# Performance work log

Measured on AMD Instinct MI355X. Metric: run time of the kernel, lower is better.

Reference implementation:

```python
import jax, jax.numpy as jnp
import numpy as np
from jax import lax

B, N, C = 16, 2048, 128
NPOINT = 512
RADII = (0.1, 0.2, 0.4)
NSAMPLES = (16, 32, 48)
C_IN = C + 3          # use_xyz: relative xyz concatenated to features
C_OUT = 128
C_MID = C_OUT // 4    # mapping_func1 out channels (non-first-layer)


def fps(xyz, npoint):
    # sequential furthest point sampling; first index is 0 (matches CUDA FPS)
    b, n, _ = xyz.shape
    def step(carry, _):
        dist, last = carry
        p = xyz[jnp.arange(b), last]                    # (B,3) last selected point
        d = jnp.sum((xyz - p[:, None, :]) ** 2, -1)     # (B,N)
        dist = jnp.minimum(dist, d)
        nxt = jnp.argmax(dist, -1).astype(jnp.int32)
        return (dist, nxt), nxt
    idx0 = jnp.zeros((b,), jnp.int32)
    (_, _), rest = lax.scan(step, (jnp.full((b, n), 1e10, jnp.float32), idx0), None, length=npoint - 1)
    return jnp.concatenate([idx0[None], rest], 0).T     # (B,npoint)


def ball_query(xyz, new_xyz, radius, nsample):
    # first `nsample` in-ball indices (in original point order), pad with first hit
    n = xyz.shape[1]
    d2 = jnp.sum((new_xyz[:, :, None, :] - xyz[:, None, :, :]) ** 2, -1)  # (B,np,N)
    scores = jnp.where(d2 < radius * radius, jnp.arange(n, dtype=jnp.int32), n)
    vals = -lax.top_k(-scores, nsample)[0]               # ascending valid indices, invalid == n
    first = vals[..., :1]                                # center is always in its own ball
    return jnp.where(vals >= n, first, vals)             # (B,np,ns) int32


def gather_points(pts, idx):
    # pts (B,N,D), idx (B,np,ns) -> (B,np,ns,D)
    return jax.vmap(lambda p, i: p[i])(pts, idx)


def sa_forward(xyz, features, W1, b1, W2, b2, Wcr, bcr):
    fi = fps(xyz, NPOINT)
    new_xyz = jax.vmap(lambda p, i: p[i])(xyz, fi)       # (B,np,3)
    featT = jnp.transpose(features, (0, 2, 1))           # (B,N,C)
    outs = []
    for r, ns in zip(RADII, NSAMPLES):
        idx = ball_query(xyz, new_xyz, r, ns)
        g_xyz = gather_points(xyz, idx)                  # (B,np,ns,3) absolute neighbor coords
        rel = g_xyz - new_xyz[:, :, None, :]             # relative coords
        gf = gather_points(featT, idx)                   # (B,np,ns,C)
        x = jnp.concatenate([rel, gf], -1)               # (B,np,ns,C_in)
        dist = jnp.linalg.norm(rel, axis=-1, keepdims=True)
        ci = jnp.broadcast_to(new_xyz[:, :, None, :], g_xyz.shape)
        h10 = jnp.concatenate([dist, ci, g_xyz, rel], -1)        # relation prior (B,np,ns,10)
        h = jax.nn.relu(h10 @ W1 + b1) @ W2 + b2                 # dynamic weights (B,np,ns,C_in)
        pooled = jnp.max(jax.nn.relu(h * x), 2)                  # (B,np,C_in) max over neighbors
        outs.append(jax.nn.relu(pooled @ Wcr + bcr))             # channel raising (B,np,C_out)
    new_features = jnp.transpose(jnp.concatenate(outs, -1), (0, 2, 1))  # (B, 3*C_out, np)
    return new_xyz, new_features


def setup_inputs() -> dict:
    key = jax.random.key(0)
    ks = jax.random.split(key, 6)
    s = 0.05
    xyz = jax.random.uniform(ks[0], (B, N, 3), jnp.float32)
    features = jax.random.normal(ks[1], (B, C, N), jnp.float32)
    W1 = jax.random.normal(ks[2], (10, C_MID), jnp.float32) * s
    b1 = jnp.zeros((C_MID,), jnp.float32)
    W2 = jax.random.normal(ks[3], (C_MID, C_IN), jnp.float32) * s
    b2 = jnp.zeros((C_IN,), jnp.float32)
    Wcr = jax.random.normal(ks[4], (C_IN, C_OUT), jnp.float32) * s
    bcr = jnp.zeros((C_OUT,), jnp.float32)
    return dict(xyz=xyz, features=features, W1=W1, b1=b1, W2=W2, b2=b2, Wcr=Wcr, bcr=bcr)


def reference(xyz, features, W1, b1, W2, b2, Wcr, bcr):
    return sa_forward(xyz, features, W1, b1, W2, b2, Wcr, bcr)
```

## Files before the change

### kernel.cpp

```cpp
#include <hip/hip_runtime.h>
#include <hip/hip_bf16.h>

#define BATCH   16
#define NPTS    2048
#define NPOINT  512
#define CFEAT   128
#define CIN     131
#define CMID    32
#define NS_TOT  96

typedef float v2f __attribute__((ext_vector_type(2)));

__device__ __forceinline__ float d2_rn(float ax, float ay, float az,
                                       float bx, float by, float bz) {
  float dx = __fsub_rn(ax, bx), dy = __fsub_rn(ay, by), dz = __fsub_rn(az, bz);
  return __fadd_rn(__fadd_rn(__fmul_rn(dx, dx), __fmul_rn(dy, dy)), __fmul_rn(dz, dz));
}

__device__ __forceinline__ unsigned long long wave_kmax64(unsigned long long k) {
#define KSTEP(CTRL, RMASK, BMASK)                                              \
  {                                                                            \
    unsigned hi = (unsigned)(k >> 32), lo = (unsigned)k;                       \
    unsigned thi = (unsigned)__builtin_amdgcn_update_dpp(                      \
        (int)hi, (int)hi, CTRL, RMASK, BMASK, false);                          \
    unsigned tlo = (unsigned)__builtin_amdgcn_update_dpp(                      \
        (int)lo, (int)lo, CTRL, RMASK, BMASK, false);                          \
    unsigned long long tk = ((unsigned long long)thi << 32) | tlo;             \
    k = tk > k ? tk : k;                                                       \
  }
  KSTEP(0x111, 0xf, 0xf)
  KSTEP(0x112, 0xf, 0xf)
  KSTEP(0x114, 0xf, 0xe)
  KSTEP(0x118, 0xf, 0xc)
  KSTEP(0x142, 0xa, 0xf)
  KSTEP(0x143, 0xc, 0xf)
#undef KSTEP
  return k;
}

__global__ __launch_bounds__(256) void fps_transpose_kernel(
    const float* __restrict__ xyz, const float* __restrict__ feat,
    float* __restrict__ featT, float* __restrict__ out_xyz)
{
  int t = threadIdx.x;
  if (blockIdx.x >= BATCH) {
    __shared__ float tile[32][33];
    int m  = blockIdx.x - BATCH;
    int b  = m >> 8;
    int c0 = ((m >> 6) & 3) << 5;
    int n0 = (m & 63) << 5;
    int tx = t & 31, ty = t >> 5;
    const float* src = feat  + (size_t)b * CFEAT * NPTS;
    float*       dst = featT + (size_t)b * NPTS * CFEAT;
#pragma unroll
    for (int i = 0; i < 4; ++i)
      tile[ty + 8 * i][tx] = src[(size_t)(c0 + ty + 8 * i) * NPTS + n0 + tx];
    __syncthreads();
#pragma unroll
    for (int i = 0; i < 4; ++i)
      dst[(size_t)(n0 + ty + 8 * i) * CFEAT + c0 + tx] = tile[tx][ty + 8 * i];
    return;
  }
  __shared__ float4 sp[NPTS];
  __shared__ unsigned long long skey[2][4];
  __shared__ int slast[NPOINT];
  int b = blockIdx.x;
  const float* xb = xyz + (size_t)b * NPTS * 3;
  for (int n = t; n < NPTS; n += 256) {
    const float* p = xb + n * 3;
    sp[n] = make_float4(p[0], p[1], p[2], 0.f);
  }
  if (t == 0) slast[0] = 0;
  __syncthreads();
  float lx[8], ly[8], lz[8], d[8];
#pragma unroll
  for (int i = 0; i < 8; ++i) {
    float4 q = sp[(i << 8) + t];
    lx[i] = q.x; ly[i] = q.y; lz[i] = q.z;
    d[i] = 1e10f;
  }
  int last = 0;
  int w = t >> 6;
  int tb = 0xFFF - t;
#pragma unroll 1
  for (int step = 1; step < NPOINT; ++step) {
    float4 pv = sp[last];
    unsigned long long best = 0ull;
#pragma unroll
    for (int i = 0; i < 8; ++i) {
      float dd = d2_rn(lx[i], ly[i], lz[i], pv.x, pv.y, pv.z);
      float nd = fminf(d[i], dd);
      d[i] = nd;
      unsigned long long k = ((unsigned long long)__float_as_uint(nd) << 32)
                           | (unsigned)(tb - (i << 8));
      best = (k > best) ? k : best;
    }
    unsigned long long wk = wave_kmax64(best);
    int par = step & 1;
    if ((t & 63) == 63) skey[par][w] = wk;
    __syncthreads();
    unsigned long long k0 = skey[par][0], k1 = skey[par][1];
    unsigned long long k2 = skey[par][2], k3 = skey[par][3];
    unsigned long long ka = k0 > k1 ? k0 : k1;
    unsigned long long kb = k2 > k3 ? k2 : k3;
    unsigned long long km = ka > kb ? ka : kb;
    last = (0xFFF - (int)((unsigned)km & 0xFFFu)) & (NPTS - 1);
    if (t == 0) slast[step] = last;
  }
  __syncthreads();
  for (int s = t; s < NPOINT; s += 256) {
    float4 q = sp[slast[s]];
    float* o = out_xyz + ((size_t)b * NPOINT + s) * 3;
    o[0] = q.x; o[1] = q.y; o[2] = q.z;
  }
}

__global__ __launch_bounds__(128, 4) void center_kernel(
    const float* __restrict__ xyz, const float* __restrict__ featT,
    const float* __restrict__ W1, const float* __restrict__ b1,
    const float* __restrict__ W2, const float* __restrict__ b2,
    const float* __restrict__ Wcr, const float* __restrict__ bcr,
    const float* __restrict__ new_xyz, float* __restrict__ out_feat)
{
  int j = blockIdx.x, b = blockIdx.y, t = threadIdx.x;
  __shared__ int   sIdx[NS_TOT];
  __shared__ __align__(16) float sH1[NS_TOT * 36];
  __shared__ float sVr[NS_TOT * 4];
  __shared__ __align__(16) float sPooled[3 * 132];

  float cx = new_xyz[((size_t)b * NPOINT + j) * 3 + 0];
  float cy = new_xyz[((size_t)b * NPOINT + j) * 3 + 1];
  float cz = new_xyz[((size_t)b * NPOINT + j) * 3 + 2];

  {
    int w = t >> 6, lane = t & 63;
    const float* xb = xyz + (size_t)b * NPTS * 3;
    unsigned long long lt = (1ull << lane) - 1ull;
    if (w == 0) {
      int c0 = 0, c1 = 0;
      for (int it = 0; it < 32; ++it) {
        int n = (it << 6) + lane;
        float px = xb[n * 3 + 0], py = xb[n * 3 + 1], pz = xb[n * 3 + 2];
        float d2 = d2_rn(cx, cy, cz, px, py, pz);
        bool i0 = d2 < 0.01f, i1 = d2 < 0.04f;
        unsigned long long m0 = __ballot(i0), m1 = __ballot(i1);
        if (i0) { int pos = c0 + __popcll(m0 & lt); if (pos < 16) sIdx[pos] = n; }
        if (i1) { int pos = c1 + __popcll(m1 & lt); if (pos < 32) sIdx[16 + pos] = n; }
        c0 += __popcll(m0); c1 += __popcll(m1);
        if (c0 >= 16 && c1 >= 32) break;
      }
      int f0 = sIdx[0];
      int f1 = sIdx[16];
      if (lane >= c0 && lane < 16) sIdx[lane] = f0;
      if (lane >= c1 && lane < 32) sIdx[16 + lane] = f1;
    } else {
      int c2 = 0;
      for (int it = 0; it < 32; ++it) {
        int n = (it << 6) + lane;
        float px = xb[n * 3 + 0], py = xb[n * 3 + 1], pz = xb[n * 3 + 2];
        float d2 = d2_rn(cx, cy, cz, px, py, pz);
        bool i2 = d2 < 0.16f;
        unsigned long long m2 = __ballot(i2);
        if (i2) { int pos = c2 + __popcll(m2 & lt); if (pos < 48) sIdx[48 + pos] = n; }
        c2 += __popcll(m2);
        if (c2 >= 48) break;
      }
      int f2 = sIdx[48];
      if (lane >= c2 && lane < 48) sIdx[48 + lane] = f2;
    }
  }
  __syncthreads();

  if (t < NS_TOT) {
    int idx = sIdx[t];
    const float* p = xyz + ((size_t)b * NPTS + (size_t)idx) * 3;
    float px = p[0], py = p[1], pz = p[2];
    float rx = __fsub_rn(px, cx), ry = __fsub_rn(py, cy), rz = __fsub_rn(pz, cz);
    float dist = sqrtf(__fadd_rn(__fadd_rn(__fmul_rn(rx, rx), __fmul_rn(ry, ry)),
                                 __fmul_rn(rz, rz)));
    float h10[10] = {dist, cx, cy, cz, px, py, pz, rx, ry, rz};
    float h1r[CMID];
#pragma unroll
    for (int m = 0; m < CMID / 2; ++m) {
      v2f a = { b1[2 * m], b1[2 * m + 1] };
#pragma unroll
      for (int i = 0; i < 10; ++i) {
        v2f wv = { W1[i * CMID + 2 * m], W1[i * CMID + 2 * m + 1] };
        v2f hv = { h10[i], h10[i] };
        a = __builtin_elementwise_fma(hv, wv, a);
      }
      v2f z = { 0.f, 0.f };
      a = __builtin_elementwise_max(a, z);
      h1r[2 * m] = a.x; h1r[2 * m + 1] = a.y;
    }
#pragma unroll
    for (int q = 0; q < 8; ++q)
      *(float4*)&sH1[t * 36 + 4 * q] = *(const float4*)&h1r[4 * q];
    v2f pa0 = { b2[0], 0.f }, pa1 = { b2[1], 0.f }, pa2 = { b2[2], 0.f };
#pragma unroll
    for (int m = 0; m < CMID / 2; ++m) {
      v2f hv = { h1r[2 * m], h1r[2 * m + 1] };
      v2f w0 = { W2[(2 * m) * CIN + 0], W2[(2 * m + 1) * CIN + 0] };
      v2f w1 = { W2[(2 * m) * CIN + 1], W2[(2 * m + 1) * CIN + 1] };
      v2f w2 = { W2[(2 * m) * CIN + 2], W2[(2 * m + 1) * CIN + 2] };
      pa0 = __builtin_elementwise_fma(hv, w0, pa0);
      pa1 = __builtin_elementwise_fma(hv, w1, pa1);
      pa2 = __builtin_elementwise_fma(hv, w2, pa2);
    }
    float a0 = __fadd_rn(pa0.x, pa0.y);
    float a1 = __fadd_rn(pa1.x, pa1.y);
    float a2 = __fadd_rn(pa2.x, pa2.y);
    sVr[t * 4 + 0] = fmaxf(__fmul_rn(a0, rx), 0.f);
    sVr[t * 4 + 1] = fmaxf(__fmul_rn(a1, ry), 0.f);
    sVr[t * 4 + 2] = fmaxf(__fmul_rn(a2, rz), 0.f);
  }
  __syncthreads();

  {
    int w = t >> 6, lane = t & 63;
    v2f wA[16], wB[16];
#pragma unroll
    for (int m = 0; m < 16; ++m) {
      wA[m] = (v2f){ W2[(2 * m) * CIN + 3 + lane],
                     W2[(2 * m + 1) * CIN + 3 + lane] };
      wB[m] = (v2f){ W2[(2 * m) * CIN + 3 + lane + 64],
                     W2[(2 * m + 1) * CIN + 3 + lane + 64] };
    }
    float bA = b2[3 + lane], bB = b2[3 + lane + 64];
    const float* ftb = featT + (size_t)b * NPTS * CFEAT;
    int sBeg = w ? 48 : 0;
    int sEnd = w ? 96 : 48;
    int sMid = w ? 10000 : 16;
    float xA0 = ftb[(size_t)sIdx[sBeg] * CFEAT + lane];
    float xB0 = ftb[(size_t)sIdx[sBeg] * CFEAT + lane + 64];
    float xA1 = ftb[(size_t)sIdx[sBeg + 1] * CFEAT + lane];
    float xB1 = ftb[(size_t)sIdx[sBeg + 1] * CFEAT + lane + 64];
    float plA = 0.f, plB = 0.f;
#pragma unroll 1
    for (int s = sBeg; s < sEnd; ++s) {
      int sp2 = (s + 2 < sEnd) ? s + 2 : sEnd - 1;
      float xA2 = ftb[(size_t)sIdx[sp2] * CFEAT + lane];
      float xB2 = ftb[(size_t)sIdx[sp2] * CFEAT + lane + 64];
      const float4* h4 = (const float4*)&sH1[s * 36];
      v2f aAA = (v2f){ bA, 0.f }, aAB = (v2f){ 0.f, 0.f };
      v2f aBA = (v2f){ bB, 0.f }, aBB = (v2f){ 0.f, 0.f };
#pragma unroll
      for (int q = 0; q < 8; ++q) {
        float4 h = h4[q];
        v2f hxy = (v2f){ h.x, h.y }, hzw = (v2f){ h.z, h.w };
        aAA = __builtin_elementwise_fma(hxy, wA[2 * q],     aAA);
        aAB = __builtin_elementwise_fma(hzw, wA[2 * q + 1], aAB);
        aBA = __builtin_elementwise_fma(hxy, wB[2 * q],     aBA);
        aBB = __builtin_elementwise_fma(hzw, wB[2 * q + 1], aBB);
      }
      float hA = __fadd_rn(__fadd_rn(aAA.x, aAA.y), __fadd_rn(aAB.x, aAB.y));
      float hB = __fadd_rn(__fadd_rn(aBA.x, aBA.y), __fadd_rn(aBB.x, aBB.y));
      plA = fmaxf(plA, fmaxf(__fmul_rn(hA, xA0), 0.f));
      plB = fmaxf(plB, fmaxf(__fmul_rn(hB, xB0), 0.f));
      xA0 = xA1; xA1 = xA2; xB0 = xB1; xB1 = xB2;
      if (s + 1 == sMid) {
        sPooled[0 * 132 + 3 + lane]      = plA;
        sPooled[0 * 132 + 3 + lane + 64] = plB;
        plA = 0.f; plB = 0.f;
      }
    }
    int rowL = w ? 2 : 1;
    sPooled[rowL * 132 + 3 + lane]      = plA;
    sPooled[rowL * 132 + 3 + lane + 64] = plB;
  }
  if (t < 9) {
    int r = t / 3, c = t - r * 3;
    int s0 = (r == 0) ? 0 : (r == 1 ? 16 : 48);
    int s1 = (r == 0) ? 16 : (r == 1 ? 48 : 96);
    float pl = 0.f;
    for (int s = s0; s < s1; ++s) pl = fmaxf(pl, sVr[s * 4 + c]);
    sPooled[r * 132 + c] = pl;
  }
  __syncthreads();

  v2f s01 = { bcr[t], bcr[t] };
  float s2 = bcr[t];
#pragma unroll 1
  for (int k4 = 0; k4 < 128; k4 += 4) {
    float4 p0 = *(const float4*)&sPooled[k4];
    float4 p1 = *(const float4*)&sPooled[132 + k4];
    float4 p2 = *(const float4*)&sPooled[264 + k4];
#pragma unroll
    for (int u = 0; u < 4; ++u) {
      float w = Wcr[(k4 + u) * CFEAT + t];
      float e0 = (&p0.x)[u], e1 = (&p1.x)[u], e2 = (&p2.x)[u];
      s01 = __builtin_elementwise_fma((v2f){ e0, e1 }, (v2f){ w, w }, s01);
      s2  = fmaf(e2, w, s2);
    }
  }
#pragma unroll
  for (int k = 128; k < CIN; ++k) {
    float w = Wcr[k * CFEAT + t];
    s01 = __builtin_elementwise_fma((v2f){ sPooled[k], sPooled[132 + k] },
                                    (v2f){ w, w }, s01);
    s2  = fmaf(sPooled[264 + k], w, s2);
  }
  float* ob = out_feat + (size_t)b * 384 * NPOINT + j;
  ob[(size_t)(0 * CFEAT + t) * NPOINT] = fmaxf(s01.x, 0.f);
  ob[(size_t)(1 * CFEAT + t) * NPOINT] = fmaxf(s01.y, 0.f);
  ob[(size_t)(2 * CFEAT + t) * NPOINT] = fmaxf(s2, 0.f);
}

extern "C" void kernel_launch(void* const* d_in, const int* in_sizes, int n_in,
                              void* d_out, int out_size, void* d_ws, size_t ws_size,
                              hipStream_t stream) {
  const float* xyz  = (const float*)d_in[0];
  const float* feat = (const float*)d_in[1];
  const float* W1   = (const float*)d_in[2];
  const float* b1   = (const float*)d_in[3];
  const float* W2   = (const float*)d_in[4];
  const float* b2   = (const float*)d_in[5];
  const float* Wcr  = (const float*)d_in[6];
  const float* bcr  = (const float*)d_in[7];
  float* out_xyz  = (float*)d_out;
  float* out_feat = out_xyz + (size_t)BATCH * NPOINT * 3;
  float* featT    = (float*)d_ws;

  fps_transpose_kernel<<<BATCH + BATCH * 256, 256, 0, stream>>>(xyz, feat, featT, out_xyz);
  center_kernel<<<dim3(NPOINT, BATCH), 128, 0, stream>>>(
      xyz, featT, W1, b1, W2, b2, Wcr, bcr, (const float*)d_out, out_feat);
}
```

Baseline: 501.6 us.

## Fuse FPS, transpose and center stages into one kernel with progress flags

Merges the FPS, feature transpose and per-center kernels into a single launch. Center blocks spin on per-batch atomic progress counters published by the FPS block every 8 steps, and on transpose completion counts, so grouping work can overlap the sequential FPS. Center blocks grow to 256 threads, splitting the neighbor loop over four waves with an extra max-reduction in shared memory. This risks spin-wait deadlock if center blocks occupy the GPU before producer blocks run (a bounded timeout guards it), lowers occupancy from the larger blocks, and adds a memset launch.

```diff
diff --git a/kernel.cpp b/kernel.cpp
--- a/kernel.cpp
+++ b/kernel.cpp
@@ -8,6 +8,9 @@
 #define CIN     131
 #define CMID    32
 #define NS_TOT  96
+#define NTRANS  (BATCH * 256)
+#define NCENT   (NPOINT * BATCH)
+#define SMEM_BYTES 34880
 
 typedef float v2f __attribute__((ext_vector_type(2)));
 
@@ -38,33 +41,14 @@
   return k;
 }
 
-__global__ __launch_bounds__(256) void fps_transpose_kernel(
-    const float* __restrict__ xyz, const float* __restrict__ feat,
-    float* __restrict__ featT, float* __restrict__ out_xyz)
+__device__ __forceinline__ void fps_body(
+    const float* __restrict__ xyz, float* __restrict__ out_xyz,
+    int* prog, int b, int t, char* smem)
 {
-  int t = threadIdx.x;
-  if (blockIdx.x >= BATCH) {
-    __shared__ float tile[32][33];
-    int m  = blockIdx.x - BATCH;
-    int b  = m >> 8;
-    int c0 = ((m >> 6) & 3) << 5;
-    int n0 = (m & 63) << 5;
-    int tx = t & 31, ty = t >> 5;
-    const float* src = feat  + (size_t)b * CFEAT * NPTS;
-    float*       dst = featT + (size_t)b * NPTS * CFEAT;
-#pragma unroll
-    for (int i = 0; i < 4; ++i)
-      tile[ty + 8 * i][tx] = src[(size_t)(c0 + ty + 8 * i) * NPTS + n0 + tx];
-    __syncthreads();
-#pragma unroll
-    for (int i = 0; i < 4; ++i)
-      dst[(size_t)(n0 + ty + 8 * i) * CFEAT + c0 + tx] = tile[tx][ty + 8 * i];
-    return;
-  }
-  __shared__ float4 sp[NPTS];
-  __shared__ unsigned long long skey[2][4];
-  __shared__ int slast[NPOINT];
-  int b = blockIdx.x;
+  float4* sp = (float4*)smem;
+  unsigned long long* skey = (unsigned long long*)(smem + 32768);
+  int* slast = (int*)(smem + 32832);
+
   const float* xb = xyz + (size_t)b * NPTS * 3;
   for (int n = t; n < NPTS; n += 256) {
     const float* p = xb + n * 3;
@@ -97,36 +81,80 @@
     }
     unsigned long long wk = wave_kmax64(best);
     int par = step & 1;
-    if ((t & 63) == 63) skey[par][w] = wk;
+    if ((t & 63) == 63) skey[par * 4 + w] = wk;
     __syncthreads();
-    unsigned long long k0 = skey[par][0], k1 = skey[par][1];
-    unsigned long long k2 = skey[par][2], k3 = skey[par][3];
+    unsigned long long k0 = skey[par * 4 + 0], k1 = skey[par * 4 + 1];
+    unsigned long long k2 = skey[par * 4 + 2], k3 = skey[par * 4 + 3];
     unsigned long long ka = k0 > k1 ? k0 : k1;
     unsigned long long kb = k2 > k3 ? k2 : k3;
     unsigned long long km = ka > kb ? ka : kb;
     last = (0xFFF - (int)((unsigned)km & 0xFFFu)) & (NPTS - 1);
     if (t == 0) slast[step] = last;
-  }
-  __syncthreads();
-  for (int s = t; s < NPOINT; s += 256) {
-    float4 q = sp[slast[s]];
-    float* o = out_xyz + ((size_t)b * NPOINT + s) * 3;
-    o[0] = q.x; o[1] = q.y; o[2] = q.z;
-  }
-}
-
-__global__ __launch_bounds__(128, 4) void center_kernel(
+    if ((step & 7) == 7) {
+      if (t < 24) {
+        int k = t / 3, c = t - k * 3;
+        int pt = slast[step - 7 + k];
+        out_xyz[((size_t)b * NPOINT + (step - 7 + k)) * 3 + c] =
+            ((const float*)&sp[pt])[c];
+      }
+      if (prog && t == 0)
+        __hip_atomic_store(prog + b, step + 1, __ATOMIC_RELEASE,
+                           __HIP_MEMORY_SCOPE_AGENT);
+    }
+  }
+}
+
+__device__ __forceinline__ void transpose_body(
+    const float* __restrict__ feat, float* __restrict__ featT,
+    int* tdone, int m, int t, char* smem)
+{
+  float (*tile)[33] = (float (*)[33])smem;
+  int b  = m >> 8;
+  int c0 = ((m >> 6) & 3) << 5;
+  int n0 = (m & 63) << 5;
+  int tx = t & 31, ty = t >> 5;
+  const float* src = feat  + (size_t)b * CFEAT * NPTS;
+  float*       dst = featT + (size_t)b * NPTS * CFEAT;
+#pragma unroll
+  for (int i = 0; i < 4; ++i)
+    tile[ty + 8 * i][tx] = src[(size_t)(c0 + ty + 8 * i) * NPTS + n0 + tx];
+  __syncthreads();
+#pragma unroll
+  for (int i = 0; i < 4; ++i)
+    dst[(size_t)(n0 + ty + 8 * i) * CFEAT + c0 + tx] = tile[tx][ty + 8 * i];
+  if (tdone) {
+    __syncthreads();
+    if (t == 0)
+      __hip_atomic_fetch_add(tdone + b, 1, __ATOMIC_RELEASE,
+                             __HIP_MEMORY_SCOPE_AGENT);
+  }
+}
+
+__device__ __forceinline__ void center_body(
     const float* __restrict__ xyz, const float* __restrict__ featT,
     const float* __restrict__ W1, const float* __restrict__ b1,
     const float* __restrict__ W2, const float* __restrict__ b2,
     const float* __restrict__ Wcr, const float* __restrict__ bcr,
-    const float* __restrict__ new_xyz, float* __restrict__ out_feat)
+    const float* __restrict__ new_xyz, float* __restrict__ out_feat,
+    int* prog, int* tdone, int b, int j, int t, char* smem)
 {
-  int j = blockIdx.x, b = blockIdx.y, t = threadIdx.x;
-  __shared__ int   sIdx[NS_TOT];
-  __shared__ __align__(16) float sH1[NS_TOT * 36];
-  __shared__ float sVr[NS_TOT * 4];
-  __shared__ __align__(16) float sPooled[3 * 132];
+  int*   sIdx    = (int*)smem;
+  float* sH1     = (float*)(smem + 384);
+  float* sVr     = (float*)(smem + 14208);
+  float* sPooled = (float*)(smem + 15744);
+  float* sP      = (float*)(smem + 17328);
+
+  if (prog) {
+    if (t == 0) {
+      int g = 0;
+      while (__hip_atomic_load(prog + b, __ATOMIC_ACQUIRE,
+                               __HIP_MEMORY_SCOPE_AGENT) <= j) {
+        __builtin_amdgcn_s_sleep(8);
+        if (++g > (1 << 20)) break;
+      }
+    }
+    __syncthreads();
+  }
 
   float cx = new_xyz[((size_t)b * NPOINT + j) * 3 + 0];
   float cy = new_xyz[((size_t)b * NPOINT + j) * 3 + 1];
@@ -153,7 +181,7 @@
       int f1 = sIdx[16];
       if (lane >= c0 && lane < 16) sIdx[lane] = f0;
       if (lane >= c1 && lane < 32) sIdx[16 + lane] = f1;
-    } else {
+    } else if (w == 1) {
       int c2 = 0;
       for (int it = 0; it < 32; ++it) {
         int n = (it << 6) + lane;
@@ -214,6 +242,16 @@
     sVr[t * 4 + 1] = fmaxf(__fmul_rn(a1, ry), 0.f);
     sVr[t * 4 + 2] = fmaxf(__fmul_rn(a2, rz), 0.f);
   }
+  if (prog) {
+    if (t == 0) {
+      int g = 0;
+      while (__hip_atomic_load(tdone + b, __ATOMIC_ACQUIRE,
+                               __HIP_MEMORY_SCOPE_AGENT) < 256) {
+        __builtin_amdgcn_s_sleep(8);
+        if (++g > (1 << 20)) break;
+      }
+    }
+  }
   __syncthreads();
 
   {
@@ -228,9 +266,7 @@
     }
     float bA = b2[3 + lane], bB = b2[3 + lane + 64];
     const float* ftb = featT + (size_t)b * NPTS * CFEAT;
-    int sBeg = w ? 48 : 0;
-    int sEnd = w ? 96 : 48;
-    int sMid = w ? 10000 : 16;
+    int sBeg = w * 24, sEnd = sBeg + 24;
     float xA0 = ftb[(size_t)sIdx[sBeg] * CFEAT + lane];
     float xB0 = ftb[(size_t)sIdx[sBeg] * CFEAT + lane + 64];
     float xA1 = ftb[(size_t)sIdx[sBeg + 1] * CFEAT + lane];
@@ -258,15 +294,14 @@
       plA = fmaxf(plA, fmaxf(__fmul_rn(hA, xA0), 0.f));
       plB = fmaxf(plB, fmaxf(__fmul_rn(hB, xB0), 0.f));
       xA0 = xA1; xA1 = xA2; xB0 = xB1; xB1 = xB2;
-      if (s + 1 == sMid) {
+      if (w == 0 && s == 15) {
         sPooled[0 * 132 + 3 + lane]      = plA;
         sPooled[0 * 132 + 3 + lane + 64] = plB;
         plA = 0.f; plB = 0.f;
       }
     }
-    int rowL = w ? 2 : 1;
-    sPooled[rowL * 132 + 3 + lane]      = plA;
-    sPooled[rowL * 132 + 3 + lane + 64] = plB;
+    sP[w * 128 + lane]      = plA;
+    sP[w * 128 + lane + 64] = plB;
   }
   if (t < 9) {
     int r = t / 3, c = t - r * 3;
@@ -277,33 +312,64 @@
     sPooled[r * 132 + c] = pl;
   }
   __syncthreads();
-
-  v2f s01 = { bcr[t], bcr[t] };
-  float s2 = bcr[t];
+  if (t < 128) {
+    sPooled[1 * 132 + 3 + t] = fmaxf(sP[0 * 128 + t], sP[1 * 128 + t]);
+    sPooled[2 * 132 + 3 + t] = fmaxf(sP[2 * 128 + t], sP[3 * 128 + t]);
+  }
+  __syncthreads();
+
+  if (t < 128) {
+    v2f s01 = { bcr[t], bcr[t] };
+    float s2 = bcr[t];
 #pragma unroll 1
-  for (int k4 = 0; k4 < 128; k4 += 4) {
-    float4 p0 = *(const float4*)&sPooled[k4];
-    float4 p1 = *(const float4*)&sPooled[132 + k4];
-    float4 p2 = *(const float4*)&sPooled[264 + k4];
-#pragma unroll
-    for (int u = 0; u < 4; ++u) {
-      float w = Wcr[(k4 + u) * CFEAT + t];
-      float e0 = (&p0.x)[u], e1 = (&p1.x)[u], e2 = (&p2.x)[u];
-      s01 = __builtin_elementwise_fma((v2f){ e0, e1 }, (v2f){ w, w }, s01);
-      s2  = fmaf(e2, w, s2);
-    }
-  }
-#pragma unroll
-  for (int k = 128; k < CIN; ++k) {
-    float w = Wcr[k * CFEAT + t];
-    s01 = __builtin_elementwise_fma((v2f){ sPooled[k], sPooled[132 + k] },
-                                    (v2f){ w, w }, s01);
-    s2  = fmaf(sPooled[264 + k], w, s2);
-  }
-  float* ob = out_feat + (size_t)b * 384 * NPOINT + j;
-  ob[(size_t)(0 * CFEAT + t) * NPOINT] = fmaxf(s01.x, 0.f);
-  ob[(size_t)(1 * CFEAT + t) * NPOINT] = fmaxf(s01.y, 0.f);
-  ob[(size_t)(2 * CFEAT + t) * NPOINT] = fmaxf(s2, 0.f);
+    for (int k4 = 0; k4 < 128; k4 += 4) {
+      float4 p0 = *(const float4*)&sPooled[k4];
+      float4 p1 = *(const float4*)&sPooled[132 + k4];
+      float4 p2 = *(const float4*)&sPooled[264 + k4];
+#pragma unroll
+      for (int u = 0; u < 4; ++u) {
+        float w = Wcr[(k4 + u) * CFEAT + t];
+        float e0 = (&p0.x)[u], e1 = (&p1.x)[u], e2 = (&p2.x)[u];
+        s01 = __builtin_elementwise_fma((v2f){ e0, e1 }, (v2f){ w, w }, s01);
+        s2  = fmaf(e2, w, s2);
+      }
+    }
+#pragma unroll
+    for (int k = 128; k < CIN; ++k) {
+      float w = Wcr[k * CFEAT + t];
+      s01 = __builtin_elementwise_fma((v2f){ sPooled[k], sPooled[132 + k] },
+                                      (v2f){ w, w }, s01);
+      s2  = fmaf(sPooled[264 + k], w, s2);
+    }
+    float* ob = out_feat + (size_t)b * 384 * NPOINT + j;
+    ob[(size_t)(0 * CFEAT + t) * NPOINT] = fmaxf(s01.x, 0.f);
+    ob[(size_t)(1 * CFEAT + t) * NPOINT] = fmaxf(s01.y, 0.f);
+    ob[(size_t)(2 * CFEAT + t) * NPOINT] = fmaxf(s2, 0.f);
+  }
+}
+
+__global__ __launch_bounds__(256) void fused_kernel(
+    const float* __restrict__ xyz, const float* __restrict__ feat,
+    const float* __restrict__ W1, const float* __restrict__ b1,
+    const float* __restrict__ W2, const float* __restrict__ b2,
+    const float* __restrict__ Wcr, const float* __restrict__ bcr,
+    float* __restrict__ featT, float* __restrict__ out_xyz,
+    float* __restrict__ out_feat, int* prog, int* tdone, int center_only)
+{
+  __shared__ __align__(16) char smem[SMEM_BYTES];
+  int t = threadIdx.x;
+  int id = blockIdx.x;
+  if (!center_only) {
+    if (id < BATCH) { fps_body(xyz, out_xyz, prog, id, t, smem); return; }
+    if (id < BATCH + NTRANS) {
+      transpose_body(feat, featT, tdone, id - BATCH, t, smem); return;
+    }
+    id -= BATCH + NTRANS;
+  }
+  int b = id & (BATCH - 1);
+  int j = id >> 4;
+  center_body(xyz, featT, W1, b1, W2, b2, Wcr, bcr, out_xyz, out_feat,
+              prog, tdone, b, j, t, smem);
 }
 
 extern "C" void kernel_launch(void* const* d_in, const int* in_sizes, int n_in,
@@ -320,8 +386,20 @@
   float* out_xyz  = (float*)d_out;
   float* out_feat = out_xyz + (size_t)BATCH * NPOINT * 3;
   float* featT    = (float*)d_ws;
-
-  fps_transpose_kernel<<<BATCH + BATCH * 256, 256, 0, stream>>>(xyz, feat, featT, out_xyz);
-  center_kernel<<<dim3(NPOINT, BATCH), 128, 0, stream>>>(
-      xyz, featT, W1, b1, W2, b2, Wcr, bcr, (const float*)d_out, out_feat);
-}
+  size_t featT_bytes = (size_t)BATCH * NPTS * CFEAT * sizeof(float);
+
+  if (ws_size >= featT_bytes + 256) {
+    int* flags = (int*)((char*)d_ws + featT_bytes);
+    hipMemsetAsync(flags, 0, 128, stream);
+    fused_kernel<<<BATCH + NTRANS + NCENT, 256, 0, stream>>>(
+        xyz, feat, W1, b1, W2, b2, Wcr, bcr, featT, out_xyz, out_feat,
+        flags, flags + 16, 0);
+  } else {
+    fused_kernel<<<BATCH + NTRANS, 256, 0, stream>>>(
+        xyz, feat, W1, b1, W2, b2, Wcr, bcr, featT, out_xyz, out_feat,
+        nullptr, nullptr, 0);
+    fused_kernel<<<NCENT, 256, 0, stream>>>(
+        xyz, feat, W1, b1, W2, b2, Wcr, bcr, featT, out_xyz, out_feat,
+        nullptr, nullptr, 1);
+  }
+}
```

Result: slower. 532.3 us (+6.1%).
